# Kernel tuning notes

Measured on AMD Instinct MI355X. Metric: run time of the kernel, lower is better.

The kernel has to match this reference:

```python
import jax, jax.numpy as jnp
import numpy as np

EPS = 1e-5


def bn_relu(h, gamma, beta):
    # BatchNorm1d in training mode (batch stats over node dim) + ReLU
    mu = jnp.mean(h, axis=0)
    var = jnp.var(h, axis=0)
    return jax.nn.relu(gamma * (h - mu) * jax.lax.rsqrt(var + EPS) + beta)


def rel_graph_conv(x, src, dst, etypes, W, loopW, bias, num_nodes):
    # transform-then-gather: cheaper than per-edge matmul since N < E
    h_all = jnp.einsum('ni,rio->rno', x, W)          # [R, N, out]
    msg = h_all[etypes, src]                          # [E, out] gather
    agg = jax.ops.segment_sum(msg, dst, num_segments=num_nodes)  # scatter-sum
    return agg + x @ loopW + bias


def setup_inputs() -> dict:
    key = jax.random.key(0)
    ks = jax.random.split(key, 10)
    N, E, R, F_in, H, L = 100000, 1600000, 4, 64, 128, 2
    s = 1.0 / np.sqrt(H)
    return {
        'x': jax.random.normal(ks[0], (N, F_in), jnp.float32),
        'src': jax.random.randint(ks[1], (E,), 0, N, jnp.int32),
        'dst': jax.random.randint(ks[2], (E,), 0, N, jnp.int32),
        'etypes': jax.random.randint(ks[3], (E,), 0, R, jnp.int32),
        'W0': jax.random.normal(ks[4], (R, F_in, H), jnp.float32) / np.sqrt(F_in),
        'loop0': jax.random.normal(ks[5], (F_in, H), jnp.float32) / np.sqrt(F_in),
        'b0': jnp.zeros((H,), jnp.float32),
        'g0': jnp.ones((H,), jnp.float32),
        'be0': jnp.zeros((H,), jnp.float32),
        'Ws': jax.random.normal(ks[6], (L, R, H, H), jnp.float32) * s,
        'loops': jax.random.normal(ks[7], (L, H, H), jnp.float32) * s,
        'bs': jnp.zeros((L, H), jnp.float32),
        'gs': jnp.ones((L, H), jnp.float32),
        'bes': jnp.zeros((L, H), jnp.float32),
        'Wl': jax.random.normal(ks[8], (H, H), jnp.float32) * s,
        'bl': jnp.zeros((H,), jnp.float32),
        'gl': jnp.ones((H,), jnp.float32),
        'bel': jnp.zeros((H,), jnp.float32),
    }


def reference(x, src, dst, etypes, W0, loop0, b0, g0, be0,
              Ws, loops, bs, gs, bes, Wl, bl, gl, bel):
    N = x.shape[0]
    h = bn_relu(rel_graph_conv(x, src, dst, etypes, W0, loop0, b0, N), g0, be0)
    for l in range(Ws.shape[0]):  # small fixed number of layers
        h = bn_relu(rel_graph_conv(h, src, dst, etypes, Ws[l], loops[l], bs[l], N), gs[l], bes[l])
    # last_layer: Linear + BatchNorm (no ReLU)
    h = h @ Wl + bl
    mu = jnp.mean(h, axis=0)
    var = jnp.var(h, axis=0)
    return gl * (h - mu) * jax.lax.rsqrt(var + EPS) + bel
```

## Files before the change

kernel.cpp:

```cpp
#include <hip/hip_runtime.h>

constexpr int H = 128;
constexpr int EPB = 8192;
constexpr int BSH = 8;
constexpr int NSHADOW = 32;

typedef __attribute__((ext_vector_type(8))) __bf16 bf16x8;
typedef __attribute__((ext_vector_type(4))) float  f32x4;

__device__ __forceinline__ unsigned short f2bf(float f) {
  unsigned u = __builtin_bit_cast(unsigned, f);
  u += 0x7FFFu + ((u >> 16) & 1u);
  return (unsigned short)(u >> 16);
}
__device__ __forceinline__ float bf2f(unsigned short b) {
  unsigned u = ((unsigned)b) << 16;
  return __builtin_bit_cast(float, u);
}

__global__ void zero_k(float* p, int n) {
  const int i = blockIdx.x * 256 + threadIdx.x;
  if (i < n) p[i] = 0.f;
}

__global__ __launch_bounds__(256) void prep_w_k(
    const float* __restrict__ Wr, const float* __restrict__ loopW,
    unsigned short* __restrict__ Bpre, int K, int colTiles, int nRel)
{
  const int idx = blockIdx.x * 256 + threadIdx.x;
  const int kSteps = K / 32;
  const int total = colTiles * kSteps * 64;
  if (idx >= total) return;
  const int lane = idx & 63;
  const int s    = (idx >> 6) % kSteps;
  const int Ct   = idx / (kSteps * 64);
  const int col  = Ct * 16 + (lane & 15);
  const int g    = col >> 7;
  const int cg   = col & 127;
  const float* src = (g < nRel) ? (Wr + (size_t)g * K * H + cg) : (loopW + cg);
  const int k0 = s * 32 + (lane >> 4) * 8;
  unsigned short v[8];
#pragma unroll
  for (int j = 0; j < 8; ++j) v[j] = f2bf(src[(size_t)(k0 + j) * H]);
  unsigned short* dst = Bpre + (size_t)(((Ct * kSteps + s) * 64 + lane)) * 8;
  *(uint4*)dst = *(uint4*)v;
}

__global__ __launch_bounds__(256) void bucket_hist_k(
    const int* __restrict__ dst, int E, int* __restrict__ gcnt, int nbuckets)
{
  __shared__ int cnt[512];
  const int tid = threadIdx.x;
  for (int b = tid; b < nbuckets; b += 256) cnt[b] = 0;
  __syncthreads();
  const int base = blockIdx.x * EPB;
  for (int j = tid; j < EPB; j += 256) {
    const int e = base + j;
    if (e < E) atomicAdd(&cnt[dst[e] >> BSH], 1);
  }
  __syncthreads();
  for (int b = tid; b < nbuckets; b += 256)
    if (cnt[b]) atomicAdd(&gcnt[b], cnt[b]);
}

__global__ __launch_bounds__(512) void bucket_scan_k(
    const int* __restrict__ gcnt, int* __restrict__ boffs,
    int* __restrict__ pcur, int nbuckets, int E)
{
  __shared__ int s[512];
  const int t = threadIdx.x;
  const int x = (t < nbuckets) ? gcnt[t] : 0;
  s[t] = x; __syncthreads();
  for (int off = 1; off < 512; off <<= 1) {
    const int v = (t >= off) ? s[t - off] : 0;
    __syncthreads(); s[t] += v; __syncthreads();
  }
  if (t < nbuckets) {
    const int excl = s[t] - x;
    boffs[t] = excl;
    pcur[t * 16] = excl;
  }
  if (t == 0) boffs[nbuckets] = E;
}

__global__ __launch_bounds__(256) void pack2_k(
    const int* __restrict__ src, const int* __restrict__ dst,
    const int* __restrict__ et, int E,
    int* __restrict__ pcur, int* __restrict__ ep_log, int nbuckets)
{
  __shared__ int cnt[512];
  __shared__ int basel[512];
  __shared__ unsigned short ranks[EPB];
  const int tid = threadIdx.x;
  for (int b = tid; b < nbuckets; b += 256) cnt[b] = 0;
  __syncthreads();
  const int base = blockIdx.x * EPB;
  for (int j = tid; j < EPB; j += 256) {
    const int e = base + j;
    if (e < E) ranks[j] = (unsigned short)atomicAdd(&cnt[dst[e] >> BSH], 1);
  }
  __syncthreads();
  for (int b = tid; b < nbuckets; b += 256)
    basel[b] = cnt[b] ? atomicAdd(&pcur[b * 16], cnt[b]) : 0;
  __syncthreads();
  for (int j = tid; j < EPB; j += 256) {
    const int e = base + j;
    if (e < E) {
      const int d = dst[e];
      const int pos = basel[d >> BSH] + ranks[j];
      ep_log[pos] = ((d & 255) << 19) | (et[e] << 17) | src[e];
    }
  }
}

__global__ __launch_bounds__(256) void bucket_sort2_k(
    const int* __restrict__ boffs, const int* __restrict__ ep_log,
    int* __restrict__ ep, int* __restrict__ rowp, int Nn, int E)
{
  __shared__ int ent[EPB];
  __shared__ int cntA[256];
  __shared__ int curA[256];
  const int b = blockIdx.x;
  const int tid = threadIdx.x;
  const int beg = boffs[b], end = boffs[b + 1];
  const int n = end - beg;
  const bool inl = (n <= EPB);
  if (inl) for (int i = tid; i < n; i += 256) ent[i] = ep_log[beg + i];
  cntA[tid] = 0;
  __syncthreads();
  for (int i = tid; i < n; i += 256) {
    const int v = inl ? ent[i] : ep_log[beg + i];
    atomicAdd(&cntA[v >> 19], 1);
  }
  __syncthreads();
  const int my = cntA[tid];
  for (int off = 1; off < 256; off <<= 1) {
    const int v = (tid >= off) ? cntA[tid - off] : 0;
    __syncthreads(); cntA[tid] += v; __syncthreads();
  }
  const int excl = cntA[tid] - my;
  const int node = (b << BSH) + tid;
  if (node < Nn) rowp[node] = beg + excl;
  if (b == 0 && tid == 0) rowp[Nn] = E;
  curA[tid] = excl;
  __syncthreads();
  for (int i = tid; i < n; i += 256) {
    const int v = inl ? ent[i] : ep_log[beg + i];
    const int p = atomicAdd(&curA[v >> 19], 1);
    ep[beg + p] = v & 0x7FFFF;
  }
}

template<int KSTEPS, int BN>
__global__ __launch_bounds__(256) void mfma_gemm_t(
    const float* __restrict__ Af,
    const unsigned short* __restrict__ Bpre,
    const float* __restrict__ bias,
    const float* __restrict__ stats,
    const float* __restrict__ gamma, const float* __restrict__ beta,
    unsigned short* __restrict__ tmp_all,
    float* __restrict__ agg,
    int M, int nGroups, int fpGroup, float invN)
{
  constexpr int K = KSTEPS * 32;
  constexpr int strideL = K + 8;
  __shared__ unsigned short Alds[128 * strideL];
  __shared__ float sbt[128], tbt[128];
  const int tid = threadIdx.x;
  const int rowBase = blockIdx.x * 128;

  if (BN) {
    if (tid < 128) {
      float su = 0.f, qu = 0.f;
#pragma unroll
      for (int c = 0; c < NSHADOW; ++c) {
        su += stats[c * 256 + tid];
        qu += stats[c * 256 + 128 + tid];
      }
      const float mu  = su * invN;
      const float var = qu * invN - mu * mu;
      const float s = gamma[tid] * rsqrtf(var + 1e-5f);
      sbt[tid] = s; tbt[tid] = beta[tid] - s * mu;
    }
    __syncthreads();
  }

  constexpr int cpr4 = K / 4;
  for (int c = tid; c < 128 * cpr4; c += 256) {
    const int row = c / cpr4;
    const int k4  = c % cpr4;
    const int grow = rowBase + row;
    float4 v = make_float4(0.f, 0.f, 0.f, 0.f);
    if (grow < M) v = *(const float4*)(Af + (size_t)grow * K + k4 * 4);
    unsigned short o[4];
    if (BN) {
      const int col = k4 * 4;
      o[0] = f2bf(fmaxf(fmaf(sbt[col+0], v.x, tbt[col+0]), 0.f));
      o[1] = f2bf(fmaxf(fmaf(sbt[col+1], v.y, tbt[col+1]), 0.f));
      o[2] = f2bf(fmaxf(fmaf(sbt[col+2], v.z, tbt[col+2]), 0.f));
      o[3] = f2bf(fmaxf(fmaf(sbt[col+3], v.w, tbt[col+3]), 0.f));
    } else {
      o[0] = f2bf(v.x); o[1] = f2bf(v.y); o[2] = f2bf(v.z); o[3] = f2bf(v.w);
    }
    *(uint2*)(Alds + (size_t)row * strideL + k4 * 4) = *(uint2*)o;
  }
  __syncthreads();

  const int wave = tid >> 6, lane = tid & 63;
  const int quad = lane >> 4, l15 = lane & 15;

  bf16x8 a[2][KSTEPS];
#pragma unroll
  for (int rt = 0; rt < 2; ++rt) {
    const int row = wave * 32 + rt * 16 + l15;
#pragma unroll
    for (int s = 0; s < KSTEPS; ++s)
      a[rt][s] = *(const bf16x8*)(Alds + (size_t)row * strideL + s * 32 + quad * 8);
  }

  for (int g = 0; g < nGroups; ++g) {
    f32x4 acc[2][8] = {};
    const unsigned short* bp = Bpre + ((size_t)g * 8) * KSTEPS * 64 * 8;
#pragma unroll
    for (int s = 0; s < KSTEPS; ++s) {
#pragma unroll
      for (int c = 0; c < 8; ++c) {
        const bf16x8 b = *(const bf16x8*)(bp + (size_t)((c * KSTEPS + s) * 64 + lane) * 8);
        acc[0][c] = __builtin_amdgcn_mfma_f32_16x16x32_bf16(a[0][s], b, acc[0][c], 0, 0, 0);
        acc[1][c] = __builtin_amdgcn_mfma_f32_16x16x32_bf16(a[1][s], b, acc[1][c], 0, 0, 0);
      }
    }
    if (g < fpGroup) {
      unsigned short* outp = tmp_all + (size_t)g * M * H;
#pragma unroll
      for (int rt = 0; rt < 2; ++rt)
#pragma unroll
        for (int reg = 0; reg < 4; ++reg) {
          const int row = rowBase + wave * 32 + rt * 16 + quad * 4 + reg;
          if (row >= M) continue;
#pragma unroll
          for (int c = 0; c < 8; ++c)
            outp[(size_t)row * H + c * 16 + l15] = f2bf(acc[rt][c][reg]);
        }
    } else {
#pragma unroll
      for (int rt = 0; rt < 2; ++rt)
#pragma unroll
        for (int reg = 0; reg < 4; ++reg) {
          const int row = rowBase + wave * 32 + rt * 16 + quad * 4 + reg;
          if (row >= M) continue;
#pragma unroll
          for (int c = 0; c < 8; ++c) {
            const int col = c * 16 + l15;
            agg[(size_t)row * H + col] = acc[rt][c][reg] + bias[col];
          }
        }
    }
  }
}

__global__ __launch_bounds__(256) void gather_csr_k(
    const unsigned short* __restrict__ tmp_all, const int* __restrict__ rowp,
    const int* __restrict__ ep, float* __restrict__ agg,
    float* __restrict__ shadow, int Nn)
{
  __shared__ float sAcc[4][128];
  __shared__ float qAcc[4][128];
  const int tid = threadIdx.x;
  const int wave = tid >> 6, lane = tid & 63;
  sAcc[wave][lane] = 0.f;  sAcc[wave][64 + lane] = 0.f;
  qAcc[wave][lane] = 0.f;  qAcc[wave][64 + lane] = 0.f;

  const int waveId = blockIdx.x * 4 + wave;
  const int nWaves = gridDim.x * 4;
  for (int node = waveId; node < Nn; node += nWaves) {
    const int beg = rowp[node];
    const int end = rowp[node + 1];
    float2 acc = ((const float2*)(agg + (size_t)node * H))[lane];
    int e = beg;
    int cnt = end - beg;
    while (cnt > 0) {
      const int take = cnt < 64 ? cnt : 64;
      const int pv = (lane < take) ? ep[e + lane] : 0;
      for (int j0 = 0; j0 < take; j0 += 8) {
        const int m = take - j0;
        int pj[8];
#pragma unroll
        for (int j = 0; j < 8; ++j) pj[j] = __shfl(pv, j0 + j);
        if (m >= 8) {
          unsigned vv[8];
#pragma unroll
          for (int j = 0; j < 8; ++j)
            vv[j] = *(const unsigned*)(tmp_all +
                ((size_t)(pj[j] >> 17) * Nn + (pj[j] & 0x1FFFF)) * H + lane * 2);
#pragma unroll
          for (int j = 0; j < 8; ++j) {
            acc.x += bf2f((unsigned short)(vv[j] & 0xFFFF));
            acc.y += bf2f((unsigned short)(vv[j] >> 16));
          }
        } else {
          for (int j = 0; j < m; ++j) {
            const unsigned v = *(const unsigned*)(tmp_all +
                ((size_t)(pj[j] >> 17) * Nn + (pj[j] & 0x1FFFF)) * H + lane * 2);
            acc.x += bf2f((unsigned short)(v & 0xFFFF));
            acc.y += bf2f((unsigned short)(v >> 16));
          }
        }
      }
      e += take; cnt -= take;
    }
    ((float2*)(agg + (size_t)node * H))[lane] = acc;
    sAcc[wave][lane * 2]     += acc.x;
    sAcc[wave][lane * 2 + 1] += acc.y;
    qAcc[wave][lane * 2]     += acc.x * acc.x;
    qAcc[wave][lane * 2 + 1] += acc.y * acc.y;
  }
  __syncthreads();
  float* sh = shadow + (size_t)(blockIdx.x & (NSHADOW - 1)) * 256;
  if (tid < 128) {
    atomicAdd(&sh[tid], sAcc[0][tid] + sAcc[1][tid] + sAcc[2][tid] + sAcc[3][tid]);
  } else {
    const int c = tid - 128;
    atomicAdd(&sh[128 + c], qAcc[0][c] + qAcc[1][c] + qAcc[2][c] + qAcc[3][c]);
  }
}

__global__ __launch_bounds__(256) void bn_stats_k(
    const float* __restrict__ X, int Nn, float* __restrict__ stats)
{
  const int col  = threadIdx.x & 127;
  const int half = threadIdx.x >> 7;
  float s = 0.f, q = 0.f;
  for (int row = blockIdx.x * 2 + half; row < Nn; row += gridDim.x * 2) {
    const float v = X[(size_t)row * H + col];
    s += v; q += v * v;
  }
  __shared__ float ls[256], lq[256];
  ls[threadIdx.x] = s; lq[threadIdx.x] = q;
  __syncthreads();
  if (threadIdx.x < 128) {
    atomicAdd(&stats[col],     ls[threadIdx.x] + ls[threadIdx.x + 128]);
    atomicAdd(&stats[H + col], lq[threadIdx.x] + lq[threadIdx.x + 128]);
  }
}

__global__ __launch_bounds__(256) void bn_apply_k(
    const float* __restrict__ X, const float* __restrict__ stats,
    const float* __restrict__ gamma, const float* __restrict__ beta,
    float* __restrict__ out_f, int Nn)
{
  const size_t i = (size_t)blockIdx.x * 256 + threadIdx.x;
  const size_t total = (size_t)Nn * H;
  if (i >= total) return;
  const int col = (int)(i & 127);
  const float mu  = stats[col] / Nn;
  const float var = stats[H + col] / Nn - mu * mu;
  const float inv = rsqrtf(var + 1e-5f);
  out_f[i] = fmaf(gamma[col] * inv, X[i] - mu, beta[col]);
}

extern "C" void kernel_launch(void* const* d_in, const int* in_sizes, int n_in,
                              void* d_out, int out_size, void* d_ws, size_t ws_size,
                              hipStream_t stream)
{
  const float* x     = (const float*)d_in[0];
  const int*   src   = (const int*)d_in[1];
  const int*   dst   = (const int*)d_in[2];
  const int*   et    = (const int*)d_in[3];
  const float* W0    = (const float*)d_in[4];
  const float* loop0 = (const float*)d_in[5];
  const float* b0    = (const float*)d_in[6];
  const float* g0    = (const float*)d_in[7];
  const float* be0   = (const float*)d_in[8];
  const float* Ws    = (const float*)d_in[9];
  const float* loops = (const float*)d_in[10];
  const float* bs    = (const float*)d_in[11];
  const float* gs    = (const float*)d_in[12];
  const float* bes   = (const float*)d_in[13];
  const float* Wl    = (const float*)d_in[14];
  const float* bl    = (const float*)d_in[15];
  const float* gl    = (const float*)d_in[16];
  const float* bel   = (const float*)d_in[17];

  const int E = in_sizes[1];
  const int F_in = 64;
  const int N = in_sizes[0] / F_in;
  const int R = in_sizes[4] / (F_in * H);
  const int L = in_sizes[9] / (R * H * H);
  const float invN = 1.0f / (float)N;

  float* outp = (float*)d_out;

  char* p = (char*)d_ws;
  auto alloc = [&](size_t bytes) { char* r = p; p += (bytes + 255) & ~size_t(255); return r; };
  const int nbuckets = (N + (1 << BSH) - 1) >> BSH;
  const int c0 = (R + 1) * 8 * (F_in / 32) * 64;
  const int ch = (R + 1) * 8 * (H / 32) * 64;
  const int cf = 8 * (H / 32) * 64;
  const int shadowN = NSHADOW * 256;
  float*          agg      = (float*)alloc((size_t)N * H * 4);
  float*          shadow   = (float*)alloc((size_t)(L + 1) * shadowN * 4);
  float*          statsF   = (float*)alloc(2 * H * 4);
  unsigned short* tmp_all  = (unsigned short*)alloc((size_t)R * N * H * 2);
  unsigned short* Bpre_all = (unsigned short*)alloc((size_t)(c0 + L * ch + cf) * 8 * 2);
  int*            gcnt     = (int*)alloc((size_t)nbuckets * 4);
  int*            boffs    = (int*)alloc((size_t)(nbuckets + 1) * 4);
  int*            pcur     = (int*)alloc((size_t)nbuckets * 16 * 4);
  int*            rowp     = (int*)alloc((size_t)(N + 1) * 4);
  int*            ep       = (int*)alloc((size_t)E * 4);
  int*            ep_log   = (int*)alloc((size_t)E * 4);
  (void)ws_size;

  const int pblocks = (E + EPB - 1) / EPB;
  const int rowBlocks = (N + 127) / 128;

  hipLaunchKernelGGL(prep_w_k, dim3((c0 + 255) / 256), dim3(256), 0, stream,
                     W0, loop0, Bpre_all, F_in, (R + 1) * 8, R);
  for (int l = 0; l < L; ++l)
    hipLaunchKernelGGL(prep_w_k, dim3((ch + 255) / 256), dim3(256), 0, stream,
                       Ws + (size_t)l * R * H * H, loops + (size_t)l * H * H,
                       Bpre_all + (size_t)(c0 + l * ch) * 8, H, (R + 1) * 8, R);
  hipLaunchKernelGGL(prep_w_k, dim3((cf + 255) / 256), dim3(256), 0, stream,
                     (const float*)nullptr, Wl, Bpre_all + (size_t)(c0 + L * ch) * 8, H, 8, 0);

  {
    const int nz = (L + 1) * shadowN + 2 * H;
    hipLaunchKernelGGL(zero_k, dim3((nz + 255) / 256), dim3(256), 0, stream, shadow, nz);
  }
  hipLaunchKernelGGL(zero_k, dim3((nbuckets + 255) / 256), dim3(256), 0, stream,
                     (float*)gcnt, nbuckets);

  hipLaunchKernelGGL(bucket_hist_k, dim3(pblocks), dim3(256), 0, stream, dst, E, gcnt, nbuckets);
  hipLaunchKernelGGL(bucket_scan_k, dim3(1), dim3(512), 0, stream, gcnt, boffs, pcur, nbuckets, E);
  hipLaunchKernelGGL(pack2_k, dim3(pblocks), dim3(256), 0, stream,
                     src, dst, et, E, pcur, ep_log, nbuckets);
  hipLaunchKernelGGL(bucket_sort2_k, dim3(nbuckets), dim3(256), 0, stream,
                     boffs, ep_log, ep, rowp, N, E);

  hipLaunchKernelGGL((mfma_gemm_t<2, 0>), dim3(rowBlocks), dim3(256), 0, stream,
                     x, Bpre_all, b0, (const float*)nullptr,
                     (const float*)nullptr, (const float*)nullptr,
                     tmp_all, agg, N, R + 1, R, invN);
  hipLaunchKernelGGL(gather_csr_k, dim3(2048), dim3(256), 0, stream,
                     tmp_all, rowp, ep, agg, shadow, N);

  for (int l = 0; l < L; ++l) {
    const float* gam = (l == 0) ? g0 : gs + (size_t)(l - 1) * H;
    const float* bet = (l == 0) ? be0 : bes + (size_t)(l - 1) * H;
    hipLaunchKernelGGL((mfma_gemm_t<4, 1>), dim3(rowBlocks), dim3(256), 0, stream,
                       agg, Bpre_all + (size_t)(c0 + l * ch) * 8, bs + (size_t)l * H,
                       shadow + (size_t)l * shadowN, gam, bet,
                       tmp_all, agg, N, R + 1, R, invN);
    hipLaunchKernelGGL(gather_csr_k, dim3(2048), dim3(256), 0, stream,
                       tmp_all, rowp, ep, agg, shadow + (size_t)(l + 1) * shadowN, N);
  }

  {
    const float* gam = (L == 0) ? g0 : gs + (size_t)(L - 1) * H;
    const float* bet = (L == 0) ? be0 : bes + (size_t)(L - 1) * H;
    hipLaunchKernelGGL((mfma_gemm_t<4, 1>), dim3(rowBlocks), dim3(256), 0, stream,
                       agg, Bpre_all + (size_t)(c0 + L * ch) * 8, bl,
                       shadow + (size_t)L * shadowN, gam, bet,
                       (unsigned short*)nullptr, agg, N, 1, 0, invN);
    hipLaunchKernelGGL(bn_stats_k, dim3(512), dim3(256), 0, stream, agg, N, statsF);
    const int apply_blocks = (int)(((size_t)N * H + 255) / 256);
    hipLaunchKernelGGL(bn_apply_k, dim3(apply_blocks), dim3(256), 0, stream,
                       agg, statsF, gl, bel, outp, N);
  }
}
```

Before: 698.9 us.

## Switch to gather-then-transform with per-relation aggregation and concatenated GEMM

Reorders each relational graph conv so that neighbour features are first summed per relation type into a concatenated bf16 buffer [N, 4*F]. A single GEMM with K=(R+1)*F then applies the relation and self-loop weights, replacing the per-relation transform, bf16 intermediate writes and gather of 128-wide rows. For layer 0 the gather reads 64-wide rows instead of 128-wide, and BN statistics move from the gather into the GEMM epilogue, followed by separate coef and apply kernels that write bf16 activations. This adds an extra pre-activation buffer pass and more kernels, and the per-edge switch on relation type may cause divergence.

```diff
diff --git a/kernel.cpp b/kernel.cpp
--- a/kernel.cpp
+++ b/kernel.cpp
@@ -17,32 +17,37 @@
   unsigned u = ((unsigned)b) << 16;
   return __builtin_bit_cast(float, u);
 }
+__device__ __forceinline__ unsigned pk2(float2 a) {
+  return (unsigned)f2bf(a.x) | ((unsigned)f2bf(a.y) << 16);
+}
 
 __global__ void zero_k(float* p, int n) {
   const int i = blockIdx.x * 256 + threadIdx.x;
   if (i < n) p[i] = 0.f;
 }
 
-__global__ __launch_bounds__(256) void prep_w_k(
+__global__ __launch_bounds__(256) void prep_wcat_k(
     const float* __restrict__ Wr, const float* __restrict__ loopW,
-    unsigned short* __restrict__ Bpre, int K, int colTiles, int nRel)
+    unsigned short* __restrict__ Bpre, int K, int segShift, int nRel)
 {
   const int idx = blockIdx.x * 256 + threadIdx.x;
-  const int kSteps = K / 32;
-  const int total = colTiles * kSteps * 64;
+  const int S = K / 32;
+  const int total = 8 * S * 64;
   if (idx >= total) return;
   const int lane = idx & 63;
-  const int s    = (idx >> 6) % kSteps;
-  const int Ct   = idx / (kSteps * 64);
+  const int s    = (idx >> 6) % S;
+  const int Ct   = idx / (S * 64);
   const int col  = Ct * 16 + (lane & 15);
-  const int g    = col >> 7;
-  const int cg   = col & 127;
-  const float* src = (g < nRel) ? (Wr + (size_t)g * K * H + cg) : (loopW + cg);
-  const int k0 = s * 32 + (lane >> 4) * 8;
+  const int k0   = s * 32 + (lane >> 4) * 8;
+  const int seg  = k0 >> segShift;
+  const int segK = 1 << segShift;
+  const int kk   = k0 & (segK - 1);
+  const float* src = (seg < nRel) ? (Wr + ((size_t)seg * segK + kk) * H + col)
+                                  : (loopW + (size_t)kk * H + col);
   unsigned short v[8];
 #pragma unroll
-  for (int j = 0; j < 8; ++j) v[j] = f2bf(src[(size_t)(k0 + j) * H]);
-  unsigned short* dst = Bpre + (size_t)(((Ct * kSteps + s) * 64 + lane)) * 8;
+  for (int j = 0; j < 8; ++j) v[j] = f2bf(src[(size_t)j * H]);
+  unsigned short* dst = Bpre + (size_t)((Ct * S + s) * 64 + lane) * 8;
   *(uint4*)dst = *(uint4*)v;
 }
 
@@ -151,212 +156,243 @@
   }
 }
 
-template<int KSTEPS, int BN>
-__global__ __launch_bounds__(256) void mfma_gemm_t(
-    const float* __restrict__ Af,
-    const unsigned short* __restrict__ Bpre,
-    const float* __restrict__ bias,
-    const float* __restrict__ stats,
-    const float* __restrict__ gamma, const float* __restrict__ beta,
-    unsigned short* __restrict__ tmp_all,
-    float* __restrict__ agg,
-    int M, int nGroups, int fpGroup, float invN)
-{
-  constexpr int K = KSTEPS * 32;
-  constexpr int strideL = K + 8;
-  __shared__ unsigned short Alds[128 * strideL];
-  __shared__ float sbt[128], tbt[128];
-  const int tid = threadIdx.x;
-  const int rowBase = blockIdx.x * 128;
-
-  if (BN) {
-    if (tid < 128) {
-      float su = 0.f, qu = 0.f;
-#pragma unroll
-      for (int c = 0; c < NSHADOW; ++c) {
-        su += stats[c * 256 + tid];
-        qu += stats[c * 256 + 128 + tid];
-      }
-      const float mu  = su * invN;
-      const float var = qu * invN - mu * mu;
-      const float s = gamma[tid] * rsqrtf(var + 1e-5f);
-      sbt[tid] = s; tbt[tid] = beta[tid] - s * mu;
-    }
-    __syncthreads();
-  }
-
-  constexpr int cpr4 = K / 4;
-  for (int c = tid; c < 128 * cpr4; c += 256) {
-    const int row = c / cpr4;
-    const int k4  = c % cpr4;
-    const int grow = rowBase + row;
-    float4 v = make_float4(0.f, 0.f, 0.f, 0.f);
-    if (grow < M) v = *(const float4*)(Af + (size_t)grow * K + k4 * 4);
-    unsigned short o[4];
-    if (BN) {
-      const int col = k4 * 4;
-      o[0] = f2bf(fmaxf(fmaf(sbt[col+0], v.x, tbt[col+0]), 0.f));
-      o[1] = f2bf(fmaxf(fmaf(sbt[col+1], v.y, tbt[col+1]), 0.f));
-      o[2] = f2bf(fmaxf(fmaf(sbt[col+2], v.z, tbt[col+2]), 0.f));
-      o[3] = f2bf(fmaxf(fmaf(sbt[col+3], v.w, tbt[col+3]), 0.f));
-    } else {
-      o[0] = f2bf(v.x); o[1] = f2bf(v.y); o[2] = f2bf(v.z); o[3] = f2bf(v.w);
-    }
-    *(uint2*)(Alds + (size_t)row * strideL + k4 * 4) = *(uint2*)o;
-  }
-  __syncthreads();
-
-  const int wave = tid >> 6, lane = tid & 63;
-  const int quad = lane >> 4, l15 = lane & 15;
-
-  bf16x8 a[2][KSTEPS];
-#pragma unroll
-  for (int rt = 0; rt < 2; ++rt) {
-    const int row = wave * 32 + rt * 16 + l15;
-#pragma unroll
-    for (int s = 0; s < KSTEPS; ++s)
-      a[rt][s] = *(const bf16x8*)(Alds + (size_t)row * strideL + s * 32 + quad * 8);
-  }
-
-  for (int g = 0; g < nGroups; ++g) {
-    f32x4 acc[2][8] = {};
-    const unsigned short* bp = Bpre + ((size_t)g * 8) * KSTEPS * 64 * 8;
-#pragma unroll
-    for (int s = 0; s < KSTEPS; ++s) {
-#pragma unroll
-      for (int c = 0; c < 8; ++c) {
-        const bf16x8 b = *(const bf16x8*)(bp + (size_t)((c * KSTEPS + s) * 64 + lane) * 8);
-        acc[0][c] = __builtin_amdgcn_mfma_f32_16x16x32_bf16(a[0][s], b, acc[0][c], 0, 0, 0);
-        acc[1][c] = __builtin_amdgcn_mfma_f32_16x16x32_bf16(a[1][s], b, acc[1][c], 0, 0, 0);
-      }
-    }
-    if (g < fpGroup) {
-      unsigned short* outp = tmp_all + (size_t)g * M * H;
-#pragma unroll
-      for (int rt = 0; rt < 2; ++rt)
-#pragma unroll
-        for (int reg = 0; reg < 4; ++reg) {
-          const int row = rowBase + wave * 32 + rt * 16 + quad * 4 + reg;
-          if (row >= M) continue;
-#pragma unroll
-          for (int c = 0; c < 8; ++c)
-            outp[(size_t)row * H + c * 16 + l15] = f2bf(acc[rt][c][reg]);
-        }
-    } else {
-#pragma unroll
-      for (int rt = 0; rt < 2; ++rt)
-#pragma unroll
-        for (int reg = 0; reg < 4; ++reg) {
-          const int row = rowBase + wave * 32 + rt * 16 + quad * 4 + reg;
-          if (row >= M) continue;
-#pragma unroll
-          for (int c = 0; c < 8; ++c) {
-            const int col = c * 16 + l15;
-            agg[(size_t)row * H + col] = acc[rt][c][reg] + bias[col];
-          }
-        }
-    }
-  }
-}
-
-__global__ __launch_bounds__(256) void gather_csr_k(
-    const unsigned short* __restrict__ tmp_all, const int* __restrict__ rowp,
-    const int* __restrict__ ep, float* __restrict__ agg,
-    float* __restrict__ shadow, int Nn)
-{
-  __shared__ float sAcc[4][128];
-  __shared__ float qAcc[4][128];
+__global__ __launch_bounds__(256) void cvt_x_k(
+    const float* __restrict__ x, unsigned short* __restrict__ xb, int nchunks)
+{
+  const int i = blockIdx.x * 256 + threadIdx.x;
+  if (i >= nchunks) return;
+  const float4 v = ((const float4*)x)[i];
+  unsigned short o[4] = { f2bf(v.x), f2bf(v.y), f2bf(v.z), f2bf(v.w) };
+  *(uint2*)(xb + (size_t)i * 4) = *(uint2*)o;
+}
+
+template<int DCOLS>
+__global__ __launch_bounds__(256) void gather4_k(
+    const unsigned short* __restrict__ hsrc,
+    const int* __restrict__ rowp, const int* __restrict__ ep,
+    unsigned short* __restrict__ aggcat,
+    int Nn)
+{
   const int tid = threadIdx.x;
   const int wave = tid >> 6, lane = tid & 63;
-  sAcc[wave][lane] = 0.f;  sAcc[wave][64 + lane] = 0.f;
-  qAcc[wave][lane] = 0.f;  qAcc[wave][64 + lane] = 0.f;
-
   const int waveId = blockIdx.x * 4 + wave;
   const int nWaves = gridDim.x * 4;
   for (int node = waveId; node < Nn; node += nWaves) {
-    const int beg = rowp[node];
-    const int end = rowp[node + 1];
-    float2 acc = ((const float2*)(agg + (size_t)node * H))[lane];
-    int e = beg;
-    int cnt = end - beg;
+    const int beg = rowp[node], end = rowp[node + 1];
+    float2 a0{0.f,0.f}, a1{0.f,0.f}, a2{0.f,0.f}, a3{0.f,0.f};
+    int e = beg, cnt = end - beg;
     while (cnt > 0) {
       const int take = cnt < 64 ? cnt : 64;
       const int pv = (lane < take) ? ep[e + lane] : 0;
       for (int j0 = 0; j0 < take; j0 += 8) {
         const int m = take - j0;
-        int pj[8];
-#pragma unroll
-        for (int j = 0; j < 8; ++j) pj[j] = __shfl(pv, j0 + j);
         if (m >= 8) {
-          unsigned vv[8];
-#pragma unroll
-          for (int j = 0; j < 8; ++j)
-            vv[j] = *(const unsigned*)(tmp_all +
-                ((size_t)(pj[j] >> 17) * Nn + (pj[j] & 0x1FFFF)) * H + lane * 2);
-#pragma unroll
-          for (int j = 0; j < 8; ++j) {
-            acc.x += bf2f((unsigned short)(vv[j] & 0xFFFF));
-            acc.y += bf2f((unsigned short)(vv[j] >> 16));
+          int pj[8];
+#pragma unroll
+          for (int j = 0; j < 8; ++j) pj[j] = __shfl(pv, j0 + j);
+          if constexpr (DCOLS == 128) {
+            unsigned vv[8];
+#pragma unroll
+            for (int j = 0; j < 8; ++j)
+              vv[j] = *(const unsigned*)(hsrc + (size_t)(pj[j] & 0x1FFFF) * DCOLS + lane * 2);
+#pragma unroll
+            for (int j = 0; j < 8; ++j) {
+              const float vx = bf2f((unsigned short)(vv[j] & 0xFFFF));
+              const float vy = bf2f((unsigned short)(vv[j] >> 16));
+              switch (pj[j] >> 17) {
+                case 0:  a0.x += vx; a0.y += vy; break;
+                case 1:  a1.x += vx; a1.y += vy; break;
+                case 2:  a2.x += vx; a2.y += vy; break;
+                default: a3.x += vx; a3.y += vy; break;
+              }
+            }
+          } else {
+            unsigned short vv[8];
+#pragma unroll
+            for (int j = 0; j < 8; ++j)
+              vv[j] = hsrc[(size_t)(pj[j] & 0x1FFFF) * DCOLS + lane];
+#pragma unroll
+            for (int j = 0; j < 8; ++j) {
+              const float vx = bf2f(vv[j]);
+              switch (pj[j] >> 17) {
+                case 0:  a0.x += vx; break;
+                case 1:  a1.x += vx; break;
+                case 2:  a2.x += vx; break;
+                default: a3.x += vx; break;
+              }
+            }
           }
         } else {
           for (int j = 0; j < m; ++j) {
-            const unsigned v = *(const unsigned*)(tmp_all +
-                ((size_t)(pj[j] >> 17) * Nn + (pj[j] & 0x1FFFF)) * H + lane * 2);
-            acc.x += bf2f((unsigned short)(v & 0xFFFF));
-            acc.y += bf2f((unsigned short)(v >> 16));
+            const int p = __shfl(pv, j0 + j);
+            const int r = p >> 17;
+            const int s = p & 0x1FFFF;
+            if constexpr (DCOLS == 128) {
+              const unsigned v = *(const unsigned*)(hsrc + (size_t)s * DCOLS + lane * 2);
+              const float vx = bf2f((unsigned short)(v & 0xFFFF));
+              const float vy = bf2f((unsigned short)(v >> 16));
+              switch (r) {
+                case 0:  a0.x += vx; a0.y += vy; break;
+                case 1:  a1.x += vx; a1.y += vy; break;
+                case 2:  a2.x += vx; a2.y += vy; break;
+                default: a3.x += vx; a3.y += vy; break;
+              }
+            } else {
+              const float vx = bf2f(hsrc[(size_t)s * DCOLS + lane]);
+              switch (r) {
+                case 0:  a0.x += vx; break;
+                case 1:  a1.x += vx; break;
+                case 2:  a2.x += vx; break;
+                default: a3.x += vx; break;
+              }
+            }
           }
         }
       }
       e += take; cnt -= take;
     }
-    ((float2*)(agg + (size_t)node * H))[lane] = acc;
-    sAcc[wave][lane * 2]     += acc.x;
-    sAcc[wave][lane * 2 + 1] += acc.y;
-    qAcc[wave][lane * 2]     += acc.x * acc.x;
-    qAcc[wave][lane * 2 + 1] += acc.y * acc.y;
-  }
-  __syncthreads();
-  float* sh = shadow + (size_t)(blockIdx.x & (NSHADOW - 1)) * 256;
+    if constexpr (DCOLS == 128) {
+      unsigned* orow = (unsigned*)(aggcat + (size_t)node * 512);
+      orow[lane]       = pk2(a0);
+      orow[64  + lane] = pk2(a1);
+      orow[128 + lane] = pk2(a2);
+      orow[192 + lane] = pk2(a3);
+    } else {
+      unsigned short* orow = aggcat + (size_t)node * 256;
+      orow[lane]       = f2bf(a0.x);
+      orow[64  + lane] = f2bf(a1.x);
+      orow[128 + lane] = f2bf(a2.x);
+      orow[192 + lane] = f2bf(a3.x);
+    }
+  }
+}
+
+template<int KTILE>
+__global__ __launch_bounds__(256) void mfma_cat_t(
+    const unsigned short* __restrict__ A0, const unsigned short* __restrict__ A1,
+    const unsigned short* __restrict__ Bpre, const float* __restrict__ bias,
+    float* __restrict__ shadow, float* __restrict__ pre,
+    int M, int W0, int D1, int nkt)
+{
+  constexpr int KS = KTILE / 32;
+  constexpr int strideL = KTILE + 8;
+  constexpr int CPR = KTILE / 8;
+  __shared__ unsigned short Alds[128 * strideL];
+  __shared__ float sred[128], qred[128];
+  const int tid = threadIdx.x;
+  const int wave = tid >> 6, lane = tid & 63;
+  const int quad = lane >> 4, l15 = lane & 15;
+  const int rowBase = blockIdx.x * 128;
+  const int S = nkt * KS;
+  if (tid < 128) { sred[tid] = 0.f; qred[tid] = 0.f; }
+
+  f32x4 acc[2][8] = {};
+  for (int kt = 0; kt < nkt; ++kt) {
+    __syncthreads();
+    for (int c = tid; c < 128 * CPR; c += 256) {
+      const int row = c / CPR, ch = c % CPR;
+      const int grow = rowBase + row;
+      const int k = kt * KTILE + ch * 8;
+      uint4 v = make_uint4(0u, 0u, 0u, 0u);
+      if (grow < M) {
+        const unsigned short* sp = (k < W0) ? (A0 + (size_t)grow * W0 + k)
+                                            : (A1 + (size_t)grow * D1 + (k - W0));
+        v = *(const uint4*)sp;
+      }
+      *(uint4*)(Alds + (size_t)row * strideL + ch * 8) = v;
+    }
+    __syncthreads();
+#pragma unroll
+    for (int s = 0; s < KS; ++s) {
+      const bf16x8 a0f = *(const bf16x8*)(Alds + (size_t)(wave * 32 + l15) * strideL + s * 32 + quad * 8);
+      const bf16x8 a1f = *(const bf16x8*)(Alds + (size_t)(wave * 32 + 16 + l15) * strideL + s * 32 + quad * 8);
+      const int sg = kt * KS + s;
+#pragma unroll
+      for (int ct = 0; ct < 8; ++ct) {
+        const bf16x8 b = *(const bf16x8*)(Bpre + (size_t)((ct * S + sg) * 64 + lane) * 8);
+        acc[0][ct] = __builtin_amdgcn_mfma_f32_16x16x32_bf16(a0f, b, acc[0][ct], 0, 0, 0);
+        acc[1][ct] = __builtin_amdgcn_mfma_f32_16x16x32_bf16(a1f, b, acc[1][ct], 0, 0, 0);
+      }
+    }
+  }
+
+  float bia[8];
+#pragma unroll
+  for (int ct = 0; ct < 8; ++ct) bia[ct] = bias[ct * 16 + l15];
+  float s8[8], q8[8];
+#pragma unroll
+  for (int ct = 0; ct < 8; ++ct) { s8[ct] = 0.f; q8[ct] = 0.f; }
+#pragma unroll
+  for (int rt = 0; rt < 2; ++rt) {
+#pragma unroll
+    for (int reg = 0; reg < 4; ++reg) {
+      const int row = rowBase + wave * 32 + rt * 16 + quad * 4 + reg;
+      if (row < M) {
+#pragma unroll
+        for (int ct = 0; ct < 8; ++ct) {
+          const float v = acc[rt][ct][reg] + bia[ct];
+          pre[(size_t)row * H + ct * 16 + l15] = v;
+          s8[ct] += v; q8[ct] += v * v;
+        }
+      }
+    }
+  }
+#pragma unroll
+  for (int ct = 0; ct < 8; ++ct) {
+    s8[ct] += __shfl_xor(s8[ct], 16); s8[ct] += __shfl_xor(s8[ct], 32);
+    q8[ct] += __shfl_xor(q8[ct], 16); q8[ct] += __shfl_xor(q8[ct], 32);
+  }
+  if (quad == 0) {
+#pragma unroll
+    for (int ct = 0; ct < 8; ++ct) {
+      atomicAdd(&sred[ct * 16 + l15], s8[ct]);
+      atomicAdd(&qred[ct * 16 + l15], q8[ct]);
+    }
+  }
+  __syncthreads();
   if (tid < 128) {
-    atomicAdd(&sh[tid], sAcc[0][tid] + sAcc[1][tid] + sAcc[2][tid] + sAcc[3][tid]);
+    float* sh = shadow + (size_t)(blockIdx.x & (NSHADOW - 1)) * 256;
+    atomicAdd(&sh[tid], sred[tid]);
+    atomicAdd(&sh[128 + tid], qred[tid]);
+  }
+}
+
+__global__ void bn_coef_k(const float* __restrict__ shadow,
+                          const float* __restrict__ gamma, const float* __restrict__ beta,
+                          float* __restrict__ st, float invN)
+{
+  const int t = threadIdx.x;
+  float su = 0.f, qu = 0.f;
+  for (int c = 0; c < NSHADOW; ++c) { su += shadow[c * 256 + t]; qu += shadow[c * 256 + 128 + t]; }
+  const float mu  = su * invN;
+  const float var = qu * invN - mu * mu;
+  const float s = gamma[t] * rsqrtf(var + 1e-5f);
+  st[t] = s; st[128 + t] = beta[t] - s * mu;
+}
+
+template<int RELU>
+__global__ __launch_bounds__(256) void bn_apply_t(
+    const float* __restrict__ pre, const float* __restrict__ st,
+    unsigned short* __restrict__ hout, float* __restrict__ fout, int nchunks)
+{
+  __shared__ float ss[128], tt[128];
+  if (threadIdx.x < 128) { ss[threadIdx.x] = st[threadIdx.x]; tt[threadIdx.x] = st[128 + threadIdx.x]; }
+  __syncthreads();
+  const int i = blockIdx.x * 256 + threadIdx.x;
+  if (i >= nchunks) return;
+  const float4 v = ((const float4*)pre)[i];
+  const int col0 = (i & 31) * 4;
+  float y0 = fmaf(ss[col0 + 0], v.x, tt[col0 + 0]);
+  float y1 = fmaf(ss[col0 + 1], v.y, tt[col0 + 1]);
+  float y2 = fmaf(ss[col0 + 2], v.z, tt[col0 + 2]);
+  float y3 = fmaf(ss[col0 + 3], v.w, tt[col0 + 3]);
+  if (RELU) {
+    unsigned short o[4] = { f2bf(fmaxf(y0, 0.f)), f2bf(fmaxf(y1, 0.f)),
+                            f2bf(fmaxf(y2, 0.f)), f2bf(fmaxf(y3, 0.f)) };
+    *(uint2*)(hout + (size_t)i * 4) = *(uint2*)o;
   } else {
-    const int c = tid - 128;
-    atomicAdd(&sh[128 + c], qAcc[0][c] + qAcc[1][c] + qAcc[2][c] + qAcc[3][c]);
-  }
-}
-
-__global__ __launch_bounds__(256) void bn_stats_k(
-    const float* __restrict__ X, int Nn, float* __restrict__ stats)
-{
-  const int col  = threadIdx.x & 127;
-  const int half = threadIdx.x >> 7;
-  float s = 0.f, q = 0.f;
-  for (int row = blockIdx.x * 2 + half; row < Nn; row += gridDim.x * 2) {
-    const float v = X[(size_t)row * H + col];
-    s += v; q += v * v;
-  }
-  __shared__ float ls[256], lq[256];
-  ls[threadIdx.x] = s; lq[threadIdx.x] = q;
-  __syncthreads();
-  if (threadIdx.x < 128) {
-    atomicAdd(&stats[col],     ls[threadIdx.x] + ls[threadIdx.x + 128]);
-    atomicAdd(&stats[H + col], lq[threadIdx.x] + lq[threadIdx.x + 128]);
-  }
-}
-
-__global__ __launch_bounds__(256) void bn_apply_k(
-    const float* __restrict__ X, const float* __restrict__ stats,
-    const float* __restrict__ gamma, const float* __restrict__ beta,
-    float* __restrict__ out_f, int Nn)
-{
-  const size_t i = (size_t)blockIdx.x * 256 + threadIdx.x;
-  const size_t total = (size_t)Nn * H;
-  if (i >= total) return;
-  const int col = (int)(i & 127);
-  const float mu  = stats[col] / Nn;
-  const float var = stats[H + col] / Nn - mu * mu;
-  const float inv = rsqrtf(var + 1e-5f);
-  out_f[i] = fmaf(gamma[col] * inv, X[i] - mu, beta[col]);
+    ((float4*)fout)[i] = make_float4(y0, y1, y2, y3);
+  }
 }
 
 extern "C" void kernel_launch(void* const* d_in, const int* in_sizes, int n_in,
@@ -394,37 +430,39 @@
   char* p = (char*)d_ws;
   auto alloc = [&](size_t bytes) { char* r = p; p += (bytes + 255) & ~size_t(255); return r; };
   const int nbuckets = (N + (1 << BSH) - 1) >> BSH;
-  const int c0 = (R + 1) * 8 * (F_in / 32) * 64;
-  const int ch = (R + 1) * 8 * (H / 32) * 64;
-  const int cf = 8 * (H / 32) * 64;
   const int shadowN = NSHADOW * 256;
-  float*          agg      = (float*)alloc((size_t)N * H * 4);
-  float*          shadow   = (float*)alloc((size_t)(L + 1) * shadowN * 4);
-  float*          statsF   = (float*)alloc(2 * H * 4);
-  unsigned short* tmp_all  = (unsigned short*)alloc((size_t)R * N * H * 2);
-  unsigned short* Bpre_all = (unsigned short*)alloc((size_t)(c0 + L * ch + cf) * 8 * 2);
+  const int c0 = 8 * (320 / 32) * 64 * 8;
+  const int ch = 8 * (640 / 32) * 64 * 8;
+  const int cf = 8 * (128 / 32) * 64 * 8;
+  float*          pre      = (float*)alloc((size_t)N * H * 4);
+  float*          shadow   = (float*)alloc((size_t)(L + 2) * shadowN * 4);
+  float*          st       = (float*)alloc((size_t)(L + 2) * 256 * 4);
+  unsigned short* aggcat   = (unsigned short*)alloc((size_t)N * 4 * H * 2);
+  unsigned short* xb       = (unsigned short*)alloc((size_t)N * F_in * 2);
+  unsigned short* hbuf     = (unsigned short*)alloc((size_t)N * H * 2);
+  unsigned short* Bpre_all = (unsigned short*)alloc((size_t)(c0 + L * ch + cf) * 2);
   int*            gcnt     = (int*)alloc((size_t)nbuckets * 4);
   int*            boffs    = (int*)alloc((size_t)(nbuckets + 1) * 4);
   int*            pcur     = (int*)alloc((size_t)nbuckets * 16 * 4);
   int*            rowp     = (int*)alloc((size_t)(N + 1) * 4);
   int*            ep       = (int*)alloc((size_t)E * 4);
-  int*            ep_log   = (int*)alloc((size_t)E * 4);
+  int*            ep_log   = (int*)pre;
   (void)ws_size;
 
   const int pblocks = (E + EPB - 1) / EPB;
   const int rowBlocks = (N + 127) / 128;
 
-  hipLaunchKernelGGL(prep_w_k, dim3((c0 + 255) / 256), dim3(256), 0, stream,
-                     W0, loop0, Bpre_all, F_in, (R + 1) * 8, R);
+  hipLaunchKernelGGL(prep_wcat_k, dim3((8 * 10 * 64 + 255) / 256), dim3(256), 0, stream,
+                     W0, loop0, Bpre_all, 320, 6, R);
   for (int l = 0; l < L; ++l)
-    hipLaunchKernelGGL(prep_w_k, dim3((ch + 255) / 256), dim3(256), 0, stream,
+    hipLaunchKernelGGL(prep_wcat_k, dim3((8 * 20 * 64 + 255) / 256), dim3(256), 0, stream,
                        Ws + (size_t)l * R * H * H, loops + (size_t)l * H * H,
-                       Bpre_all + (size_t)(c0 + l * ch) * 8, H, (R + 1) * 8, R);
-  hipLaunchKernelGGL(prep_w_k, dim3((cf + 255) / 256), dim3(256), 0, stream,
-                     (const float*)nullptr, Wl, Bpre_all + (size_t)(c0 + L * ch) * 8, H, 8, 0);
+                       Bpre_all + (size_t)(c0 + l * ch), 640, 7, R);
+  hipLaunchKernelGGL(prep_wcat_k, dim3((8 * 4 * 64 + 255) / 256), dim3(256), 0, stream,
+                     (const float*)nullptr, Wl, Bpre_all + (size_t)(c0 + L * ch), 128, 7, 0);
 
   {
-    const int nz = (L + 1) * shadowN + 2 * H;
+    const int nz = (L + 2) * shadowN;
     hipLaunchKernelGGL(zero_k, dim3((nz + 255) / 256), dim3(256), 0, stream, shadow, nz);
   }
   hipLaunchKernelGGL(zero_k, dim3((nbuckets + 255) / 256), dim3(256), 0, stream,
@@ -437,34 +475,38 @@
   hipLaunchKernelGGL(bucket_sort2_k, dim3(nbuckets), dim3(256), 0, stream,
                      boffs, ep_log, ep, rowp, N, E);
 
-  hipLaunchKernelGGL((mfma_gemm_t<2, 0>), dim3(rowBlocks), dim3(256), 0, stream,
-                     x, Bpre_all, b0, (const float*)nullptr,
-                     (const float*)nullptr, (const float*)nullptr,
-                     tmp_all, agg, N, R + 1, R, invN);
-  hipLaunchKernelGGL(gather_csr_k, dim3(2048), dim3(256), 0, stream,
-                     tmp_all, rowp, ep, agg, shadow, N);
+  hipLaunchKernelGGL(cvt_x_k, dim3((N * 16 + 255) / 256), dim3(256), 0, stream,
+                     x, xb, N * 16);
+
+  const int applyBlocks = (N * 32 + 255) / 256;
+
+  hipLaunchKernelGGL((gather4_k<64>), dim3(2048), dim3(256), 0, stream,
+                     xb, rowp, ep, aggcat, N);
+  hipLaunchKernelGGL((mfma_cat_t<64>), dim3(rowBlocks), dim3(256), 0, stream,
+                     aggcat, xb, Bpre_all, b0, shadow, pre, N, 4 * F_in, F_in, 5);
+  hipLaunchKernelGGL(bn_coef_k, dim3(1), dim3(128), 0, stream, shadow, g0, be0, st, invN);
+  hipLaunchKernelGGL((bn_apply_t<1>), dim3(applyBlocks), dim3(256), 0, stream,
+                     pre, st, hbuf, (float*)nullptr, N * 32);
 
   for (int l = 0; l < L; ++l) {
-    const float* gam = (l == 0) ? g0 : gs + (size_t)(l - 1) * H;
-    const float* bet = (l == 0) ? be0 : bes + (size_t)(l - 1) * H;
-    hipLaunchKernelGGL((mfma_gemm_t<4, 1>), dim3(rowBlocks), dim3(256), 0, stream,
-                       agg, Bpre_all + (size_t)(c0 + l * ch) * 8, bs + (size_t)l * H,
-                       shadow + (size_t)l * shadowN, gam, bet,
-                       tmp_all, agg, N, R + 1, R, invN);
-    hipLaunchKernelGGL(gather_csr_k, dim3(2048), dim3(256), 0, stream,
-                       tmp_all, rowp, ep, agg, shadow + (size_t)(l + 1) * shadowN, N);
-  }
-
-  {
-    const float* gam = (L == 0) ? g0 : gs + (size_t)(L - 1) * H;
-    const float* bet = (L == 0) ? be0 : bes + (size_t)(L - 1) * H;
-    hipLaunchKernelGGL((mfma_gemm_t<4, 1>), dim3(rowBlocks), dim3(256), 0, stream,
-                       agg, Bpre_all + (size_t)(c0 + L * ch) * 8, bl,
-                       shadow + (size_t)L * shadowN, gam, bet,
-                       (unsigned short*)nullptr, agg, N, 1, 0, invN);
-    hipLaunchKernelGGL(bn_stats_k, dim3(512), dim3(256), 0, stream, agg, N, statsF);
-    const int apply_blocks = (int)(((size_t)N * H + 255) / 256);
-    hipLaunchKernelGGL(bn_apply_k, dim3(apply_blocks), dim3(256), 0, stream,
-                       agg, statsF, gl, bel, outp, N);
-  }
-}
+    hipLaunchKernelGGL((gather4_k<128>), dim3(2048), dim3(256), 0, stream,
+                       hbuf, rowp, ep, aggcat, N);
+    hipLaunchKernelGGL((mfma_cat_t<128>), dim3(rowBlocks), dim3(256), 0, stream,
+                       aggcat, hbuf, Bpre_all + (size_t)(c0 + l * ch), bs + (size_t)l * H,
+                       shadow + (size_t)(1 + l) * shadowN, pre, N, 4 * H, H, 5);
+    hipLaunchKernelGGL(bn_coef_k, dim3(1), dim3(128), 0, stream,
+                       shadow + (size_t)(1 + l) * shadowN, gs + (size_t)l * H, bes + (size_t)l * H,
+                       st + (size_t)(1 + l) * 256, invN);
+    hipLaunchKernelGGL((bn_apply_t<1>), dim3(applyBlocks), dim3(256), 0, stream,
+                       pre, st + (size_t)(1 + l) * 256, hbuf, (float*)nullptr, N * 32);
+  }
+
+  hipLaunchKernelGGL((mfma_cat_t<128>), dim3(rowBlocks), dim3(256), 0, stream,
+                     (const unsigned short*)nullptr, hbuf, Bpre_all + (size_t)(c0 + L * ch), bl,
+                     shadow + (size_t)(1 + L) * shadowN, pre, N, 0, H, 1);
+  hipLaunchKernelGGL(bn_coef_k, dim3(1), dim3(128), 0, stream,
+                     shadow + (size_t)(1 + L) * shadowN, gl, bel,
+                     st + (size_t)(1 + L) * 256, invN);
+  hipLaunchKernelGGL((bn_apply_t<0>), dim3(applyBlocks), dim3(256), 0, stream,
+                     pre, st + (size_t)(1 + L) * 256, (unsigned short*)nullptr, outp, N * 32);
+}
```

After: 932.2 us. 33.4% more time.
